# Kernel tuning notes

Hardware: AMD Instinct MI355X
Metric: run time of the kernel (lower is better)

Reference implementation:

```python
import jax, jax.numpy as jnp
import numpy as np


def setup_inputs() -> dict:
    key = jax.random.key(0)
    k1, k2, k3 = jax.random.split(key, 3)
    B, S_enc, S_dec, D = 8, 4096, 4096, 128
    b = jax.random.normal(k1, (B, S_enc, D), dtype=jnp.float32)
    h = jax.random.normal(k2, (B, S_dec, D), dtype=jnp.float32)
    W_b = jax.random.normal(k3, (D, D), dtype=jnp.float32) * (1.0 / np.sqrt(D))
    return {"b": b, "h": h, "W_b": W_b}


def reference(b, h, W_b):
    # tmp1 = h @ W_b : [B, S_dec, D]
    tmp1 = jnp.einsum('btd,de->bte', h, W_b)
    # scores = tmp1 @ b^T : [B, S_dec, S_enc]
    scores = jnp.einsum('bte,bse->bts', tmp1, b)
    attn = jax.nn.softmax(scores, axis=-1)
    # weighted sum over encoder positions (the original does this via a huge
    # tile/broadcast/multiply/reduce_sum; math is a batched matmul)
    cxt = jnp.einsum('bts,bsd->btd', attn, b)
    return cxt
```

## Files before the change

### kernel.cpp

```cpp
#include <hip/hip_runtime.h>

typedef _Float16 half2v __attribute__((ext_vector_type(2)));
typedef _Float16 half4 __attribute__((ext_vector_type(4)));
typedef _Float16 half8 __attribute__((ext_vector_type(8)));
typedef float floatx4 __attribute__((ext_vector_type(4)));

#define B_   8
#define SE   4096
#define SD   4096
#define D_   128
#define NT   64
#define LDB  136
#define LOG2E 1.44269504f

__device__ __forceinline__ void cp16_async(const _Float16* g, _Float16* l) {
    __builtin_amdgcn_global_load_lds((const __attribute__((address_space(1))) unsigned int*)g,
                                     (__attribute__((address_space(3))) unsigned int*)l, 16, 0, 0);
}

__global__ __launch_bounds__(256) void wprep(const float* __restrict__ W,
                                             _Float16* __restrict__ W16,
                                             _Float16* __restrict__ Wlo) {
    int i = blockIdx.x * 256 + threadIdx.x;
    float w = W[i];
    _Float16 hi = (_Float16)w;
    W16[i] = hi;
    Wlo[i] = (_Float16)(w - (float)hi);
}

__global__ __launch_bounds__(256) void kvprep(const float* __restrict__ b,
                                              const _Float16* __restrict__ W16,
                                              const _Float16* __restrict__ Wlo,
                                              _Float16* __restrict__ kp,
                                              _Float16* __restrict__ vT) {
    __shared__ _Float16 bs[64 * LDB];
    const int bb = blockIdx.y, s0 = blockIdx.x * 64;
    const int tid = threadIdx.x, wave = tid >> 6, lane = tid & 63;
    const int l15 = lane & 15, quad = lane >> 4;

    const float* bg = b + ((size_t)bb * SE + s0) * D_;
    #pragma unroll
    for (int it = 0; it < 4; ++it) {
        int idx = tid + it * 256;
        int row = idx >> 4, seg = idx & 15;
        const float* src = bg + row * D_ + seg * 8;
        float4 a = *(const float4*)src;
        float4 c = *(const float4*)(src + 4);
        half8 hv;
        hv[0] = (_Float16)a.x; hv[1] = (_Float16)a.y; hv[2] = (_Float16)a.z; hv[3] = (_Float16)a.w;
        hv[4] = (_Float16)c.x; hv[5] = (_Float16)c.y; hv[6] = (_Float16)c.z; hv[7] = (_Float16)c.w;
        *(half8*)(bs + row * LDB + seg * 8) = hv;
    }
    __syncthreads();

    half8 af[4];
    #pragma unroll
    for (int ks = 0; ks < 4; ++ks)
        af[ks] = *(const half8*)(bs + (wave * 16 + l15) * LDB + ks * 32 + quad * 8);
    floatx4 acc[8];
    #pragma unroll
    for (int nt = 0; nt < 8; ++nt) acc[nt] = (floatx4){0.f, 0.f, 0.f, 0.f};
    #pragma unroll
    for (int ks = 0; ks < 4; ++ks) {
        #pragma unroll
        for (int nt = 0; nt < 8; ++nt) {
            half8 bh = *(const half8*)(W16 + (size_t)(nt * 16 + l15) * 128 + ks * 32 + quad * 8);
            half8 bl = *(const half8*)(Wlo + (size_t)(nt * 16 + l15) * 128 + ks * 32 + quad * 8);
            acc[nt] = __builtin_amdgcn_mfma_f32_16x16x32_f16(af[ks], bh, acc[nt], 0, 0, 0);
            acc[nt] = __builtin_amdgcn_mfma_f32_16x16x32_f16(af[ks], bl, acc[nt], 0, 0, 0);
        }
    }

    {
        const int sq = tid & 15, dg = tid >> 4;
        half8 rowv[4];
        #pragma unroll
        for (int j = 0; j < 4; ++j)
            rowv[j] = *(const half8*)(bs + (sq * 4 + j) * LDB + dg * 8);
        #pragma unroll
        for (int r = 0; r < 8; ++r) {
            int d = dg * 8 + r;
            half4 o;
            #pragma unroll
            for (int j = 0; j < 4; ++j) o[j] = rowv[j][r];
            *(half4*)(vT + ((size_t)bb * D_ + d) * SE + s0 + sq * 4) = o;
        }
    }
    __syncthreads();

    #pragma unroll
    for (int nt = 0; nt < 8; ++nt)
        #pragma unroll
        for (int r = 0; r < 4; ++r)
            bs[(wave * 16 + quad * 4 + r) * LDB + nt * 16 + l15] = (_Float16)acc[nt][r];
    __syncthreads();
    _Float16* kg = kp + ((size_t)bb * SE + s0) * D_;
    {
        const int row = tid >> 2;
        #pragma unroll
        for (int it = 0; it < 4; ++it) {
            int ch = (tid & 3) + it * 4;
            half8 v = *(const half8*)(bs + row * LDB + ch * 8);
            *(half8*)(kg + row * D_ + ch * 8) = v;
        }
    }
}

__global__ __launch_bounds__(256, 2) void flash(const float* __restrict__ h,
                                                const _Float16* __restrict__ k,
                                                const _Float16* __restrict__ vT,
                                                float* __restrict__ out) {
    __shared__ _Float16 KV[2][16384];

    const int bb   = blockIdx.y;
    const int q0   = blockIdx.x * 64;
    const int tid  = threadIdx.x;
    const int wave = tid >> 6;
    const int wq   = wave >> 1;
    const int ws   = wave & 1;
    const int lane = tid & 63;
    const int l15  = lane & 15;
    const int quad = lane >> 4;

    const _Float16* kbase = k + (size_t)bb * SE * D_;
    const _Float16* vbase = vT + (size_t)bb * D_ * SE;

    int koff[4], voff[4];
    #pragma unroll
    for (int j = 0; j < 4; ++j) {
        int i = (wave * 4 + j) * 64 + lane;
        int kr = i >> 4, kpp = i & 15;
        koff[j] = kr * D_ + (kpp ^ (kr & 15)) * 8;
        int vr = i >> 3, vpp = i & 7;
        voff[j] = vr * SE + (vpp ^ (vr & 7)) * 8;
    }

    const _Float16* kA0[4]; const _Float16* kA1[4];
    const _Float16* vB0[2]; const _Float16* vB1[2];
    #pragma unroll
    for (int ks = 0; ks < 4; ++ks) {
        int o = l15 * 128 + (((ks * 4 + quad) ^ l15) * 8) + ws * 4096;
        kA0[ks] = &KV[0][o]; kA1[ks] = &KV[1][o];
    }
    #pragma unroll
    for (int stl = 0; stl < 2; ++stl) {
        int o = 8192 + l15 * 64 + (((ws * 4 + stl * 2 + (quad >> 1)) ^ (l15 & 7)) * 8) + (quad & 1) * 4;
        vB0[stl] = &KV[0][o]; vB1[stl] = &KV[1][o];
    }

    {
        _Float16* buf0 = &KV[0][0];
        #pragma unroll
        for (int j = 0; j < 4; ++j) {
            cp16_async(kbase + koff[j], buf0 + (wave * 4 + j) * 512);
            cp16_async(vbase + voff[j], buf0 + 8192 + (wave * 4 + j) * 512);
        }
    }

    half8 qf[2][4];
    #pragma unroll
    for (int qt = 0; qt < 2; ++qt) {
        const float* hrow = h + ((size_t)bb * SD + q0 + wq * 32 + qt * 16 + l15) * D_;
        #pragma unroll
        for (int ks = 0; ks < 4; ++ks) {
            float4 a = *(const float4*)(hrow + ks * 32 + quad * 8);
            float4 c = *(const float4*)(hrow + ks * 32 + quad * 8 + 4);
            half8 f;
            f[0] = (_Float16)(a.x * LOG2E); f[1] = (_Float16)(a.y * LOG2E);
            f[2] = (_Float16)(a.z * LOG2E); f[3] = (_Float16)(a.w * LOG2E);
            f[4] = (_Float16)(c.x * LOG2E); f[5] = (_Float16)(c.y * LOG2E);
            f[6] = (_Float16)(c.z * LOG2E); f[7] = (_Float16)(c.w * LOG2E);
            qf[qt][ks] = f;
        }
    }

    floatx4 acc_o[2][8];
    #pragma unroll
    for (int qt = 0; qt < 2; ++qt)
        #pragma unroll
        for (int dt = 0; dt < 8; ++dt) acc_o[qt][dt] = (floatx4){0.f, 0.f, 0.f, 0.f};
    float m_q[2] = {-1e30f, -1e30f};
    float l_part[2] = {0.f, 0.f};
    const half2v one2 = { (_Float16)1.f, (_Float16)1.f };

    for (int t = 0; t < SE / NT; ++t) {
        __syncthreads();
        if (t + 1 < SE / NT) {
            const _Float16* kt = kbase + (size_t)(t + 1) * (NT * D_);
            const _Float16* vt = vbase + (size_t)(t + 1) * NT;
            _Float16* bufn = &KV[(t + 1) & 1][0];
            #pragma unroll
            for (int j = 0; j < 4; ++j) {
                cp16_async(kt + koff[j], bufn + (wave * 4 + j) * 512);
                cp16_async(vt + voff[j], bufn + 8192 + (wave * 4 + j) * 512);
            }
        }
        const bool odd = (t & 1) != 0;
        const _Float16* kA[4]; const _Float16* vB[2];
        #pragma unroll
        for (int i = 0; i < 4; ++i) kA[i] = odd ? kA1[i] : kA0[i];
        #pragma unroll
        for (int i = 0; i < 2; ++i) vB[i] = odd ? vB1[i] : vB0[i];

        floatx4 accs[2][2];
        #pragma unroll
        for (int stl = 0; stl < 2; ++stl)
            #pragma unroll
            for (int qt = 0; qt < 2; ++qt) accs[stl][qt] = (floatx4){0.f, 0.f, 0.f, 0.f};
        #pragma unroll
        for (int ks = 0; ks < 4; ++ks) {
            half8 af0 = *(const half8*)(kA[ks]);
            half8 af1 = *(const half8*)(kA[ks] + 2048);
            accs[0][0] = __builtin_amdgcn_mfma_f32_16x16x32_f16(af0, qf[0][ks], accs[0][0], 0, 0, 0);
            accs[0][1] = __builtin_amdgcn_mfma_f32_16x16x32_f16(af0, qf[1][ks], accs[0][1], 0, 0, 0);
            accs[1][0] = __builtin_amdgcn_mfma_f32_16x16x32_f16(af1, qf[0][ks], accs[1][0], 0, 0, 0);
            accs[1][1] = __builtin_amdgcn_mfma_f32_16x16x32_f16(af1, qf[1][ks], accs[1][1], 0, 0, 0);
        }

        float mv[2];
        #pragma unroll
        for (int qt = 0; qt < 2; ++qt) {
            float a = fmaxf(fmaxf(accs[0][qt][0], accs[0][qt][1]), fmaxf(accs[0][qt][2], accs[0][qt][3]));
            float b2 = fmaxf(fmaxf(accs[1][qt][0], accs[1][qt][1]), fmaxf(accs[1][qt][2], accs[1][qt][3]));
            mv[qt] = fmaxf(a, b2);
        }
        bool cond = (mv[0] > m_q[0] + 11.5f) || (mv[1] > m_q[1] + 11.5f);
        if (__ballot(cond) != 0ull) {
            #pragma unroll
            for (int qt = 0; qt < 2; ++qt) {
                float m = mv[qt];
                m = fmaxf(m, __shfl_xor(m, 16, 64));
                m = fmaxf(m, __shfl_xor(m, 32, 64));
                float mnew = fmaxf(m_q[qt], m);
                float alpha = exp2f(m_q[qt] - mnew);
                l_part[qt] *= alpha;
                float ab[4];
                #pragma unroll
                for (int r = 0; r < 4; ++r) ab[r] = __shfl(alpha, quad * 4 + r, 64);
                #pragma unroll
                for (int dt = 0; dt < 8; ++dt)
                    #pragma unroll
                    for (int r = 0; r < 4; ++r) acc_o[qt][dt][r] *= ab[r];
                m_q[qt] = mnew;
            }
        }

        half4 pf[2][2];
        #pragma unroll
        for (int qt = 0; qt < 2; ++qt)
            #pragma unroll
            for (int stl = 0; stl < 2; ++stl) {
                float p0 = exp2f(accs[stl][qt][0] - m_q[qt]);
                float p1 = exp2f(accs[stl][qt][1] - m_q[qt]);
                float p2 = exp2f(accs[stl][qt][2] - m_q[qt]);
                float p3 = exp2f(accs[stl][qt][3] - m_q[qt]);
                half2v lo = __builtin_bit_cast(half2v, __builtin_amdgcn_cvt_pkrtz(p0, p1));
                half2v hi = __builtin_bit_cast(half2v, __builtin_amdgcn_cvt_pkrtz(p2, p3));
#if __has_builtin(__builtin_amdgcn_fdot2)
                l_part[qt] = __builtin_amdgcn_fdot2(lo, one2, l_part[qt], false);
                l_part[qt] = __builtin_amdgcn_fdot2(hi, one2, l_part[qt], false);
#else
                l_part[qt] += p0 + p1 + p2 + p3;
#endif
                half4 pv; pv[0] = lo[0]; pv[1] = lo[1]; pv[2] = hi[0]; pv[3] = hi[1];
                pf[qt][stl] = pv;
            }

        #pragma unroll
        for (int stl = 0; stl < 2; ++stl) {
            #pragma unroll
            for (int dt = 0; dt < 8; ++dt) {
                half4 vf = *(const half4*)(vB[stl] + dt * 1024);
                acc_o[0][dt] = __builtin_amdgcn_mfma_f32_16x16x16f16(pf[0][stl], vf, acc_o[0][dt], 0, 0, 0);
                acc_o[1][dt] = __builtin_amdgcn_mfma_f32_16x16x16f16(pf[1][stl], vf, acc_o[1][dt], 0, 0, 0);
            }
        }
    }

    float l_own[2];
    #pragma unroll
    for (int qt = 0; qt < 2; ++qt) {
        float l = l_part[qt];
        l += __shfl_xor(l, 16, 64);
        l += __shfl_xor(l, 32, 64);
        l_own[qt] = l;
    }

    __syncthreads();
    float* Ob = (float*)&KV[0][0];
    float* ml = (float*)&KV[0][0] + 8192;

    if (ws == 1) {
        #pragma unroll
        for (int qt = 0; qt < 2; ++qt) {
            #pragma unroll
            for (int dt = 0; dt < 8; ++dt)
                *(floatx4*)(Ob + (((wq * 2 + qt) * 8 + dt) * 64 + lane) * 4) = acc_o[qt][dt];
            if (quad == 0)
                *(float2*)(ml + (wq * 32 + qt * 16 + l15) * 2) = make_float2(m_q[qt], l_own[qt]);
        }
    }
    __syncthreads();
    if (ws == 0) {
        #pragma unroll
        for (int qt = 0; qt < 2; ++qt) {
            float m0r[4], l0r[4], m1r[4], l1r[4];
            #pragma unroll
            for (int r = 0; r < 4; ++r) {
                m0r[r] = __shfl(m_q[qt], quad * 4 + r, 64);
                l0r[r] = __shfl(l_own[qt], quad * 4 + r, 64);
                float2 p = *(float2*)(ml + (wq * 32 + qt * 16 + quad * 4 + r) * 2);
                m1r[r] = p.x; l1r[r] = p.y;
            }
            float a0[4], a1[4], inv[4];
            #pragma unroll
            for (int r = 0; r < 4; ++r) {
                float mm = fmaxf(m0r[r], m1r[r]);
                a0[r] = exp2f(m0r[r] - mm);
                a1[r] = exp2f(m1r[r] - mm);
                inv[r] = 1.f / (l0r[r] * a0[r] + l1r[r] * a1[r]);
            }
            float* orow = out + ((size_t)bb * SD + q0 + wq * 32 + qt * 16 + quad * 4) * D_;
            #pragma unroll
            for (int dt = 0; dt < 8; ++dt) {
                floatx4 o1 = *(floatx4*)(Ob + (((wq * 2 + qt) * 8 + dt) * 64 + lane) * 4);
                #pragma unroll
                for (int r = 0; r < 4; ++r)
                    orow[(size_t)r * D_ + dt * 16 + l15] =
                        (acc_o[qt][dt][r] * a0[r] + o1[r] * a1[r]) * inv[r];
            }
        }
    }
}

extern "C" void kernel_launch(void* const* d_in, const int* in_sizes, int n_in,
                              void* d_out, int out_size, void* d_ws, size_t ws_size,
                              hipStream_t stream) {
    const float* b = (const float*)d_in[0];
    const float* h = (const float*)d_in[1];
    const float* W = (const float*)d_in[2];
    float* out = (float*)d_out;

    _Float16* W16 = (_Float16*)d_ws;
    _Float16* Wlo = W16 + 128 * 128;
    _Float16* kp  = Wlo + 128 * 128;
    _Float16* vT  = kp + (size_t)B_ * SE * D_;

    wprep<<<64, 256, 0, stream>>>(W, W16, Wlo);
    kvprep<<<dim3(SE / 64, B_), 256, 0, stream>>>(b, W16, Wlo, kp, vT);
    flash<<<dim3(SD / 64, B_), 256, 0, stream>>>(h, kp, vT, out);
}
```

Measured before the change: 215.9 us.

## Use 512-thread flash blocks with one 16-row query tile per wave

Restructures the flash kernel so each block runs 8 waves, with each wave owning a single 16-row query tile instead of two. Register state per wave drops (acc_o, qf, m/l), so more waves can be resident, and the K/V tile loads are split across twice as many threads. The cost is that each K/V fragment read from LDS now feeds only one query tile instead of two, doubling LDS read traffic per MFMA. The block barrier also has to synchronize 8 waves.

```diff
diff --git a/kernel.cpp b/kernel.cpp
--- a/kernel.cpp
+++ b/kernel.cpp
@@ -106,7 +106,7 @@
     }
 }
 
-__global__ __launch_bounds__(256, 2) void flash(const float* __restrict__ h,
+__global__ __launch_bounds__(512, 4) void flash(const float* __restrict__ h,
                                                 const _Float16* __restrict__ k,
                                                 const _Float16* __restrict__ vT,
                                                 float* __restrict__ out) {
@@ -125,14 +125,14 @@
     const _Float16* kbase = k + (size_t)bb * SE * D_;
     const _Float16* vbase = vT + (size_t)bb * D_ * SE;
 
-    int koff[4], voff[4];
-    #pragma unroll
-    for (int j = 0; j < 4; ++j) {
-        int i = (wave * 4 + j) * 64 + lane;
+    int koff[2], voff[2];
+    #pragma unroll
+    for (int it = 0; it < 2; ++it) {
+        int i = it * 512 + wave * 64 + lane;
         int kr = i >> 4, kpp = i & 15;
-        koff[j] = kr * D_ + (kpp ^ (kr & 15)) * 8;
+        koff[it] = kr * D_ + (kpp ^ (kr & 15)) * 8;
         int vr = i >> 3, vpp = i & 7;
-        voff[j] = vr * SE + (vpp ^ (vr & 7)) * 8;
+        voff[it] = vr * SE + (vpp ^ (vr & 7)) * 8;
     }
 
     const _Float16* kA0[4]; const _Float16* kA1[4];
@@ -151,16 +151,15 @@
     {
         _Float16* buf0 = &KV[0][0];
         #pragma unroll
-        for (int j = 0; j < 4; ++j) {
-            cp16_async(kbase + koff[j], buf0 + (wave * 4 + j) * 512);
-            cp16_async(vbase + voff[j], buf0 + 8192 + (wave * 4 + j) * 512);
-        }
-    }
-
-    half8 qf[2][4];
-    #pragma unroll
-    for (int qt = 0; qt < 2; ++qt) {
-        const float* hrow = h + ((size_t)bb * SD + q0 + wq * 32 + qt * 16 + l15) * D_;
+        for (int it = 0; it < 2; ++it) {
+            cp16_async(kbase + koff[it], buf0 + (it * 512 + wave * 64) * 8);
+            cp16_async(vbase + voff[it], buf0 + 8192 + (it * 512 + wave * 64) * 8);
+        }
+    }
+
+    half8 qf[4];
+    {
+        const float* hrow = h + ((size_t)bb * SD + q0 + wq * 16 + l15) * D_;
         #pragma unroll
         for (int ks = 0; ks < 4; ++ks) {
             float4 a = *(const float4*)(hrow + ks * 32 + quad * 8);
@@ -170,17 +169,15 @@
             f[2] = (_Float16)(a.z * LOG2E); f[3] = (_Float16)(a.w * LOG2E);
             f[4] = (_Float16)(c.x * LOG2E); f[5] = (_Float16)(c.y * LOG2E);
             f[6] = (_Float16)(c.z * LOG2E); f[7] = (_Float16)(c.w * LOG2E);
-            qf[qt][ks] = f;
-        }
-    }
-
-    floatx4 acc_o[2][8];
-    #pragma unroll
-    for (int qt = 0; qt < 2; ++qt)
-        #pragma unroll
-        for (int dt = 0; dt < 8; ++dt) acc_o[qt][dt] = (floatx4){0.f, 0.f, 0.f, 0.f};
-    float m_q[2] = {-1e30f, -1e30f};
-    float l_part[2] = {0.f, 0.f};
+            qf[ks] = f;
+        }
+    }
+
+    floatx4 acc_o[8];
+    #pragma unroll
+    for (int dt = 0; dt < 8; ++dt) acc_o[dt] = (floatx4){0.f, 0.f, 0.f, 0.f};
+    float m_q = -1e30f;
+    float l_part = 0.f;
     const half2v one2 = { (_Float16)1.f, (_Float16)1.f };
 
     for (int t = 0; t < SE / NT; ++t) {
@@ -190,145 +187,121 @@
             const _Float16* vt = vbase + (size_t)(t + 1) * NT;
             _Float16* bufn = &KV[(t + 1) & 1][0];
             #pragma unroll
-            for (int j = 0; j < 4; ++j) {
-                cp16_async(kt + koff[j], bufn + (wave * 4 + j) * 512);
-                cp16_async(vt + voff[j], bufn + 8192 + (wave * 4 + j) * 512);
+            for (int it = 0; it < 2; ++it) {
+                cp16_async(kt + koff[it], bufn + (it * 512 + wave * 64) * 8);
+                cp16_async(vt + voff[it], bufn + 8192 + (it * 512 + wave * 64) * 8);
             }
         }
         const bool odd = (t & 1) != 0;
-        const _Float16* kA[4]; const _Float16* vB[2];
-        #pragma unroll
-        for (int i = 0; i < 4; ++i) kA[i] = odd ? kA1[i] : kA0[i];
-        #pragma unroll
-        for (int i = 0; i < 2; ++i) vB[i] = odd ? vB1[i] : vB0[i];
-
-        floatx4 accs[2][2];
-        #pragma unroll
-        for (int stl = 0; stl < 2; ++stl)
-            #pragma unroll
-            for (int qt = 0; qt < 2; ++qt) accs[stl][qt] = (floatx4){0.f, 0.f, 0.f, 0.f};
+        const _Float16* vB[2];
+        vB[0] = odd ? vB1[0] : vB0[0];
+        vB[1] = odd ? vB1[1] : vB0[1];
+
+        floatx4 accs[2];
+        accs[0] = (floatx4){0.f, 0.f, 0.f, 0.f};
+        accs[1] = (floatx4){0.f, 0.f, 0.f, 0.f};
         #pragma unroll
         for (int ks = 0; ks < 4; ++ks) {
-            half8 af0 = *(const half8*)(kA[ks]);
-            half8 af1 = *(const half8*)(kA[ks] + 2048);
-            accs[0][0] = __builtin_amdgcn_mfma_f32_16x16x32_f16(af0, qf[0][ks], accs[0][0], 0, 0, 0);
-            accs[0][1] = __builtin_amdgcn_mfma_f32_16x16x32_f16(af0, qf[1][ks], accs[0][1], 0, 0, 0);
-            accs[1][0] = __builtin_amdgcn_mfma_f32_16x16x32_f16(af1, qf[0][ks], accs[1][0], 0, 0, 0);
-            accs[1][1] = __builtin_amdgcn_mfma_f32_16x16x32_f16(af1, qf[1][ks], accs[1][1], 0, 0, 0);
-        }
-
-        float mv[2];
-        #pragma unroll
-        for (int qt = 0; qt < 2; ++qt) {
-            float a = fmaxf(fmaxf(accs[0][qt][0], accs[0][qt][1]), fmaxf(accs[0][qt][2], accs[0][qt][3]));
-            float b2 = fmaxf(fmaxf(accs[1][qt][0], accs[1][qt][1]), fmaxf(accs[1][qt][2], accs[1][qt][3]));
-            mv[qt] = fmaxf(a, b2);
-        }
-        bool cond = (mv[0] > m_q[0] + 11.5f) || (mv[1] > m_q[1] + 11.5f);
-        if (__ballot(cond) != 0ull) {
-            #pragma unroll
-            for (int qt = 0; qt < 2; ++qt) {
-                float m = mv[qt];
-                m = fmaxf(m, __shfl_xor(m, 16, 64));
-                m = fmaxf(m, __shfl_xor(m, 32, 64));
-                float mnew = fmaxf(m_q[qt], m);
-                float alpha = exp2f(m_q[qt] - mnew);
-                l_part[qt] *= alpha;
-                float ab[4];
+            const _Float16* ka = odd ? kA1[ks] : kA0[ks];
+            half8 af0 = *(const half8*)(ka);
+            half8 af1 = *(const half8*)(ka + 2048);
+            accs[0] = __builtin_amdgcn_mfma_f32_16x16x32_f16(af0, qf[ks], accs[0], 0, 0, 0);
+            accs[1] = __builtin_amdgcn_mfma_f32_16x16x32_f16(af1, qf[ks], accs[1], 0, 0, 0);
+        }
+
+        float mv = fmaxf(fmaxf(fmaxf(accs[0][0], accs[0][1]), fmaxf(accs[0][2], accs[0][3])),
+                         fmaxf(fmaxf(accs[1][0], accs[1][1]), fmaxf(accs[1][2], accs[1][3])));
+        if (__ballot(mv > m_q + 11.5f) != 0ull) {
+            float m = mv;
+            m = fmaxf(m, __shfl_xor(m, 16, 64));
+            m = fmaxf(m, __shfl_xor(m, 32, 64));
+            float mnew = fmaxf(m_q, m);
+            float alpha = exp2f(m_q - mnew);
+            l_part *= alpha;
+            float ab[4];
+            #pragma unroll
+            for (int r = 0; r < 4; ++r) ab[r] = __shfl(alpha, quad * 4 + r, 64);
+            #pragma unroll
+            for (int dt = 0; dt < 8; ++dt)
                 #pragma unroll
-                for (int r = 0; r < 4; ++r) ab[r] = __shfl(alpha, quad * 4 + r, 64);
-                #pragma unroll
-                for (int dt = 0; dt < 8; ++dt)
-                    #pragma unroll
-                    for (int r = 0; r < 4; ++r) acc_o[qt][dt][r] *= ab[r];
-                m_q[qt] = mnew;
-            }
-        }
-
-        half4 pf[2][2];
-        #pragma unroll
-        for (int qt = 0; qt < 2; ++qt)
-            #pragma unroll
-            for (int stl = 0; stl < 2; ++stl) {
-                float p0 = exp2f(accs[stl][qt][0] - m_q[qt]);
-                float p1 = exp2f(accs[stl][qt][1] - m_q[qt]);
-                float p2 = exp2f(accs[stl][qt][2] - m_q[qt]);
-                float p3 = exp2f(accs[stl][qt][3] - m_q[qt]);
-                half2v lo = __builtin_bit_cast(half2v, __builtin_amdgcn_cvt_pkrtz(p0, p1));
-                half2v hi = __builtin_bit_cast(half2v, __builtin_amdgcn_cvt_pkrtz(p2, p3));
+                for (int r = 0; r < 4; ++r) acc_o[dt][r] *= ab[r];
+            m_q = mnew;
+        }
+
+        half4 pf[2];
+        #pragma unroll
+        for (int stl = 0; stl < 2; ++stl) {
+            float p0 = exp2f(accs[stl][0] - m_q);
+            float p1 = exp2f(accs[stl][1] - m_q);
+            float p2 = exp2f(accs[stl][2] - m_q);
+            float p3 = exp2f(accs[stl][3] - m_q);
+            half2v lo = __builtin_bit_cast(half2v, __builtin_amdgcn_cvt_pkrtz(p0, p1));
+            half2v hi = __builtin_bit_cast(half2v, __builtin_amdgcn_cvt_pkrtz(p2, p3));
 #if __has_builtin(__builtin_amdgcn_fdot2)
-                l_part[qt] = __builtin_amdgcn_fdot2(lo, one2, l_part[qt], false);
-                l_part[qt] = __builtin_amdgcn_fdot2(hi, one2, l_part[qt], false);
+            l_part = __builtin_amdgcn_fdot2(lo, one2, l_part, false);
+            l_part = __builtin_amdgcn_fdot2(hi, one2, l_part, false);
 #else
-                l_part[qt] += p0 + p1 + p2 + p3;
+            l_part += p0 + p1 + p2 + p3;
 #endif
-                half4 pv; pv[0] = lo[0]; pv[1] = lo[1]; pv[2] = hi[0]; pv[3] = hi[1];
-                pf[qt][stl] = pv;
-            }
+            half4 pv; pv[0] = lo[0]; pv[1] = lo[1]; pv[2] = hi[0]; pv[3] = hi[1];
+            pf[stl] = pv;
+        }
 
         #pragma unroll
         for (int stl = 0; stl < 2; ++stl) {
             #pragma unroll
             for (int dt = 0; dt < 8; ++dt) {
                 half4 vf = *(const half4*)(vB[stl] + dt * 1024);
-                acc_o[0][dt] = __builtin_amdgcn_mfma_f32_16x16x16f16(pf[0][stl], vf, acc_o[0][dt], 0, 0, 0);
-                acc_o[1][dt] = __builtin_amdgcn_mfma_f32_16x16x16f16(pf[1][stl], vf, acc_o[1][dt], 0, 0, 0);
+                acc_o[dt] = __builtin_amdgcn_mfma_f32_16x16x16f16(pf[stl], vf, acc_o[dt], 0, 0, 0);
             }
         }
     }
 
-    float l_own[2];
-    #pragma unroll
-    for (int qt = 0; qt < 2; ++qt) {
-        float l = l_part[qt];
+    float l_own;
+    {
+        float l = l_part;
         l += __shfl_xor(l, 16, 64);
         l += __shfl_xor(l, 32, 64);
-        l_own[qt] = l;
+        l_own = l;
     }
 
     __syncthreads();
     float* Ob = (float*)&KV[0][0];
-    float* ml = (float*)&KV[0][0] + 8192;
+    float* ml = (float*)&KV[1][0];
 
     if (ws == 1) {
         #pragma unroll
-        for (int qt = 0; qt < 2; ++qt) {
-            #pragma unroll
-            for (int dt = 0; dt < 8; ++dt)
-                *(floatx4*)(Ob + (((wq * 2 + qt) * 8 + dt) * 64 + lane) * 4) = acc_o[qt][dt];
-            if (quad == 0)
-                *(float2*)(ml + (wq * 32 + qt * 16 + l15) * 2) = make_float2(m_q[qt], l_own[qt]);
-        }
+        for (int dt = 0; dt < 8; ++dt)
+            *(floatx4*)(Ob + ((wq * 8 + dt) * 64 + lane) * 4) = acc_o[dt];
+        if (quad == 0)
+            *(float2*)(ml + (wq * 16 + l15) * 2) = make_float2(m_q, l_own);
     }
     __syncthreads();
     if (ws == 0) {
-        #pragma unroll
-        for (int qt = 0; qt < 2; ++qt) {
-            float m0r[4], l0r[4], m1r[4], l1r[4];
-            #pragma unroll
-            for (int r = 0; r < 4; ++r) {
-                m0r[r] = __shfl(m_q[qt], quad * 4 + r, 64);
-                l0r[r] = __shfl(l_own[qt], quad * 4 + r, 64);
-                float2 p = *(float2*)(ml + (wq * 32 + qt * 16 + quad * 4 + r) * 2);
-                m1r[r] = p.x; l1r[r] = p.y;
-            }
-            float a0[4], a1[4], inv[4];
-            #pragma unroll
-            for (int r = 0; r < 4; ++r) {
-                float mm = fmaxf(m0r[r], m1r[r]);
-                a0[r] = exp2f(m0r[r] - mm);
-                a1[r] = exp2f(m1r[r] - mm);
-                inv[r] = 1.f / (l0r[r] * a0[r] + l1r[r] * a1[r]);
-            }
-            float* orow = out + ((size_t)bb * SD + q0 + wq * 32 + qt * 16 + quad * 4) * D_;
-            #pragma unroll
-            for (int dt = 0; dt < 8; ++dt) {
-                floatx4 o1 = *(floatx4*)(Ob + (((wq * 2 + qt) * 8 + dt) * 64 + lane) * 4);
-                #pragma unroll
-                for (int r = 0; r < 4; ++r)
-                    orow[(size_t)r * D_ + dt * 16 + l15] =
-                        (acc_o[qt][dt][r] * a0[r] + o1[r] * a1[r]) * inv[r];
-            }
+        float m0r[4], l0r[4], m1r[4], l1r[4];
+        #pragma unroll
+        for (int r = 0; r < 4; ++r) {
+            m0r[r] = __shfl(m_q, quad * 4 + r, 64);
+            l0r[r] = __shfl(l_own, quad * 4 + r, 64);
+            float2 p = *(float2*)(ml + (wq * 16 + quad * 4 + r) * 2);
+            m1r[r] = p.x; l1r[r] = p.y;
+        }
+        float a0[4], a1[4], inv[4];
+        #pragma unroll
+        for (int r = 0; r < 4; ++r) {
+            float mm = fmaxf(m0r[r], m1r[r]);
+            a0[r] = exp2f(m0r[r] - mm);
+            a1[r] = exp2f(m1r[r] - mm);
+            inv[r] = 1.f / (l0r[r] * a0[r] + l1r[r] * a1[r]);
+        }
+        float* orow = out + ((size_t)bb * SD + q0 + wq * 16 + quad * 4) * D_;
+        #pragma unroll
+        for (int dt = 0; dt < 8; ++dt) {
+            floatx4 o1 = *(floatx4*)(Ob + ((wq * 8 + dt) * 64 + lane) * 4);
+            #pragma unroll
+            for (int r = 0; r < 4; ++r)
+                orow[(size_t)r * D_ + dt * 16 + l15] =
+                    (acc_o[dt][r] * a0[r] + o1[r] * a1[r]) * inv[r];
         }
     }
 }
@@ -348,5 +321,5 @@
 
     wprep<<<64, 256, 0, stream>>>(W, W16, Wlo);
     kvprep<<<dim3(SE / 64, B_), 256, 0, stream>>>(b, W16, Wlo, kp, vT);
-    flash<<<dim3(SD / 64, B_), 256, 0, stream>>>(h, kp, vT, out);
-}
+    flash<<<dim3(SD / 64, B_), 512, 0, stream>>>(h, kp, vT, out);
+}
```

Measured after the change: 208.5 us. 3.4% less time.

## Split each KV tile across four waves per query group with 512-thread blocks

Applied to the files above, without the earlier changes.

The flash kernel moves from 256 to 512 threads per block, and each query group's 64-key tile is now split across four waves of 16 keys each instead of two waves of 32. Per-wave work per iteration halves, and more waves are available to hide latency and overlap MFMA with the exp/softmax work. The final merge now combines four partial softmax states through shared memory, processed one query subtile at a time, which adds more barriers and a larger reduction. Launch bounds of (512, 4) constrain registers per thread, which the 2x8 output accumulators may strain.

```diff
diff --git a/kernel.cpp b/kernel.cpp
--- a/kernel.cpp
+++ b/kernel.cpp
@@ -106,18 +106,19 @@
     }
 }
 
-__global__ __launch_bounds__(256, 2) void flash(const float* __restrict__ h,
+__global__ __launch_bounds__(512, 4) void flash(const float* __restrict__ h,
                                                 const _Float16* __restrict__ k,
                                                 const _Float16* __restrict__ vT,
                                                 float* __restrict__ out) {
     __shared__ _Float16 KV[2][16384];
+    __shared__ float mlbuf[2][4][16][2];
 
     const int bb   = blockIdx.y;
     const int q0   = blockIdx.x * 64;
     const int tid  = threadIdx.x;
     const int wave = tid >> 6;
-    const int wq   = wave >> 1;
-    const int ws   = wave & 1;
+    const int wq   = wave >> 2;
+    const int ws   = wave & 3;
     const int lane = tid & 63;
     const int l15  = lane & 15;
     const int quad = lane >> 4;
@@ -125,35 +126,34 @@
     const _Float16* kbase = k + (size_t)bb * SE * D_;
     const _Float16* vbase = vT + (size_t)bb * D_ * SE;
 
-    int koff[4], voff[4];
-    #pragma unroll
-    for (int j = 0; j < 4; ++j) {
-        int i = (wave * 4 + j) * 64 + lane;
+    int koff[2], voff[2];
+    #pragma unroll
+    for (int it = 0; it < 2; ++it) {
+        int i = it * 512 + wave * 64 + lane;
         int kr = i >> 4, kpp = i & 15;
-        koff[j] = kr * D_ + (kpp ^ (kr & 15)) * 8;
+        koff[it] = kr * D_ + (kpp ^ (kr & 15)) * 8;
         int vr = i >> 3, vpp = i & 7;
-        voff[j] = vr * SE + (vpp ^ (vr & 7)) * 8;
+        voff[it] = vr * SE + (vpp ^ (vr & 7)) * 8;
     }
 
     const _Float16* kA0[4]; const _Float16* kA1[4];
-    const _Float16* vB0[2]; const _Float16* vB1[2];
+    const _Float16* vB0;    const _Float16* vB1;
     #pragma unroll
     for (int ks = 0; ks < 4; ++ks) {
-        int o = l15 * 128 + (((ks * 4 + quad) ^ l15) * 8) + ws * 4096;
+        int o = (ws * 16 + l15) * 128 + (((ks * 4 + quad) ^ l15) * 8);
         kA0[ks] = &KV[0][o]; kA1[ks] = &KV[1][o];
     }
-    #pragma unroll
-    for (int stl = 0; stl < 2; ++stl) {
-        int o = 8192 + l15 * 64 + (((ws * 4 + stl * 2 + (quad >> 1)) ^ (l15 & 7)) * 8) + (quad & 1) * 4;
-        vB0[stl] = &KV[0][o]; vB1[stl] = &KV[1][o];
+    {
+        int o = 8192 + l15 * 64 + (((2 * ws + (quad >> 1)) ^ (l15 & 7)) * 8) + (quad & 1) * 4;
+        vB0 = &KV[0][o]; vB1 = &KV[1][o];
     }
 
     {
         _Float16* buf0 = &KV[0][0];
         #pragma unroll
-        for (int j = 0; j < 4; ++j) {
-            cp16_async(kbase + koff[j], buf0 + (wave * 4 + j) * 512);
-            cp16_async(vbase + voff[j], buf0 + 8192 + (wave * 4 + j) * 512);
+        for (int it = 0; it < 2; ++it) {
+            cp16_async(kbase + koff[it], buf0 + (it * 512 + wave * 64) * 8);
+            cp16_async(vbase + voff[it], buf0 + 8192 + (it * 512 + wave * 64) * 8);
         }
     }
 
@@ -190,40 +190,28 @@
             const _Float16* vt = vbase + (size_t)(t + 1) * NT;
             _Float16* bufn = &KV[(t + 1) & 1][0];
             #pragma unroll
-            for (int j = 0; j < 4; ++j) {
-                cp16_async(kt + koff[j], bufn + (wave * 4 + j) * 512);
-                cp16_async(vt + voff[j], bufn + 8192 + (wave * 4 + j) * 512);
+            for (int it = 0; it < 2; ++it) {
+                cp16_async(kt + koff[it], bufn + (it * 512 + wave * 64) * 8);
+                cp16_async(vt + voff[it], bufn + 8192 + (it * 512 + wave * 64) * 8);
             }
         }
         const bool odd = (t & 1) != 0;
-        const _Float16* kA[4]; const _Float16* vB[2];
-        #pragma unroll
-        for (int i = 0; i < 4; ++i) kA[i] = odd ? kA1[i] : kA0[i];
-        #pragma unroll
-        for (int i = 0; i < 2; ++i) vB[i] = odd ? vB1[i] : vB0[i];
-
-        floatx4 accs[2][2];
-        #pragma unroll
-        for (int stl = 0; stl < 2; ++stl)
-            #pragma unroll
-            for (int qt = 0; qt < 2; ++qt) accs[stl][qt] = (floatx4){0.f, 0.f, 0.f, 0.f};
+        const _Float16* vB = odd ? vB1 : vB0;
+
+        floatx4 accs[2];
+        accs[0] = (floatx4){0.f, 0.f, 0.f, 0.f};
+        accs[1] = (floatx4){0.f, 0.f, 0.f, 0.f};
         #pragma unroll
         for (int ks = 0; ks < 4; ++ks) {
-            half8 af0 = *(const half8*)(kA[ks]);
-            half8 af1 = *(const half8*)(kA[ks] + 2048);
-            accs[0][0] = __builtin_amdgcn_mfma_f32_16x16x32_f16(af0, qf[0][ks], accs[0][0], 0, 0, 0);
-            accs[0][1] = __builtin_amdgcn_mfma_f32_16x16x32_f16(af0, qf[1][ks], accs[0][1], 0, 0, 0);
-            accs[1][0] = __builtin_amdgcn_mfma_f32_16x16x32_f16(af1, qf[0][ks], accs[1][0], 0, 0, 0);
-            accs[1][1] = __builtin_amdgcn_mfma_f32_16x16x32_f16(af1, qf[1][ks], accs[1][1], 0, 0, 0);
+            half8 af = *(const half8*)(odd ? kA1[ks] : kA0[ks]);
+            accs[0] = __builtin_amdgcn_mfma_f32_16x16x32_f16(af, qf[0][ks], accs[0], 0, 0, 0);
+            accs[1] = __builtin_amdgcn_mfma_f32_16x16x32_f16(af, qf[1][ks], accs[1], 0, 0, 0);
         }
 
         float mv[2];
         #pragma unroll
-        for (int qt = 0; qt < 2; ++qt) {
-            float a = fmaxf(fmaxf(accs[0][qt][0], accs[0][qt][1]), fmaxf(accs[0][qt][2], accs[0][qt][3]));
-            float b2 = fmaxf(fmaxf(accs[1][qt][0], accs[1][qt][1]), fmaxf(accs[1][qt][2], accs[1][qt][3]));
-            mv[qt] = fmaxf(a, b2);
-        }
+        for (int qt = 0; qt < 2; ++qt)
+            mv[qt] = fmaxf(fmaxf(accs[qt][0], accs[qt][1]), fmaxf(accs[qt][2], accs[qt][3]));
         bool cond = (mv[0] > m_q[0] + 11.5f) || (mv[1] > m_q[1] + 11.5f);
         if (__ballot(cond) != 0ull) {
             #pragma unroll
@@ -245,35 +233,30 @@
             }
         }
 
-        half4 pf[2][2];
-        #pragma unroll
-        for (int qt = 0; qt < 2; ++qt)
-            #pragma unroll
-            for (int stl = 0; stl < 2; ++stl) {
-                float p0 = exp2f(accs[stl][qt][0] - m_q[qt]);
-                float p1 = exp2f(accs[stl][qt][1] - m_q[qt]);
-                float p2 = exp2f(accs[stl][qt][2] - m_q[qt]);
-                float p3 = exp2f(accs[stl][qt][3] - m_q[qt]);
-                half2v lo = __builtin_bit_cast(half2v, __builtin_amdgcn_cvt_pkrtz(p0, p1));
-                half2v hi = __builtin_bit_cast(half2v, __builtin_amdgcn_cvt_pkrtz(p2, p3));
+        half4 pf[2];
+        #pragma unroll
+        for (int qt = 0; qt < 2; ++qt) {
+            float p0 = exp2f(accs[qt][0] - m_q[qt]);
+            float p1 = exp2f(accs[qt][1] - m_q[qt]);
+            float p2 = exp2f(accs[qt][2] - m_q[qt]);
+            float p3 = exp2f(accs[qt][3] - m_q[qt]);
+            half2v lo = __builtin_bit_cast(half2v, __builtin_amdgcn_cvt_pkrtz(p0, p1));
+            half2v hi = __builtin_bit_cast(half2v, __builtin_amdgcn_cvt_pkrtz(p2, p3));
 #if __has_builtin(__builtin_amdgcn_fdot2)
-                l_part[qt] = __builtin_amdgcn_fdot2(lo, one2, l_part[qt], false);
-                l_part[qt] = __builtin_amdgcn_fdot2(hi, one2, l_part[qt], false);
+            l_part[qt] = __builtin_amdgcn_fdot2(lo, one2, l_part[qt], false);
+            l_part[qt] = __builtin_amdgcn_fdot2(hi, one2, l_part[qt], false);
 #else
-                l_part[qt] += p0 + p1 + p2 + p3;
+            l_part[qt] += p0 + p1 + p2 + p3;
 #endif
-                half4 pv; pv[0] = lo[0]; pv[1] = lo[1]; pv[2] = hi[0]; pv[3] = hi[1];
-                pf[qt][stl] = pv;
-            }
-
-        #pragma unroll
-        for (int stl = 0; stl < 2; ++stl) {
-            #pragma unroll
-            for (int dt = 0; dt < 8; ++dt) {
-                half4 vf = *(const half4*)(vB[stl] + dt * 1024);
-                acc_o[0][dt] = __builtin_amdgcn_mfma_f32_16x16x16f16(pf[0][stl], vf, acc_o[0][dt], 0, 0, 0);
-                acc_o[1][dt] = __builtin_amdgcn_mfma_f32_16x16x16f16(pf[1][stl], vf, acc_o[1][dt], 0, 0, 0);
-            }
+            half4 pv; pv[0] = lo[0]; pv[1] = lo[1]; pv[2] = hi[0]; pv[3] = hi[1];
+            pf[qt] = pv;
+        }
+
+        #pragma unroll
+        for (int dt = 0; dt < 8; ++dt) {
+            half4 vf = *(const half4*)(vB + dt * 1024);
+            acc_o[0][dt] = __builtin_amdgcn_mfma_f32_16x16x16f16(pf[0], vf, acc_o[0][dt], 0, 0, 0);
+            acc_o[1][dt] = __builtin_amdgcn_mfma_f32_16x16x16f16(pf[1], vf, acc_o[1][dt], 0, 0, 0);
         }
     }
 
@@ -286,48 +269,52 @@
         l_own[qt] = l;
     }
 
-    __syncthreads();
     float* Ob = (float*)&KV[0][0];
-    float* ml = (float*)&KV[0][0] + 8192;
-
-    if (ws == 1) {
-        #pragma unroll
-        for (int qt = 0; qt < 2; ++qt) {
+
+    #pragma unroll
+    for (int qt = 0; qt < 2; ++qt) {
+        __syncthreads();
+        if (ws != 0) {
+            float* reg = Ob + (wq * 3 + (ws - 1)) * 2048;
             #pragma unroll
             for (int dt = 0; dt < 8; ++dt)
-                *(floatx4*)(Ob + (((wq * 2 + qt) * 8 + dt) * 64 + lane) * 4) = acc_o[qt][dt];
-            if (quad == 0)
-                *(float2*)(ml + (wq * 32 + qt * 16 + l15) * 2) = make_float2(m_q[qt], l_own[qt]);
-        }
-    }
-    __syncthreads();
-    if (ws == 0) {
-        #pragma unroll
-        for (int qt = 0; qt < 2; ++qt) {
-            float m0r[4], l0r[4], m1r[4], l1r[4];
+                *(floatx4*)(reg + (dt * 64 + lane) * 4) = acc_o[qt][dt];
+            if (quad == 0) {
+                mlbuf[wq][ws][l15][0] = m_q[qt];
+                mlbuf[wq][ws][l15][1] = l_own[qt];
+            }
+        }
+        __syncthreads();
+        if (ws == 0) {
+            float m0 = m_q[qt],           l0 = l_own[qt];
+            float m1 = mlbuf[wq][1][l15][0], l1 = mlbuf[wq][1][l15][1];
+            float m2 = mlbuf[wq][2][l15][0], l2 = mlbuf[wq][2][l15][1];
+            float m3 = mlbuf[wq][3][l15][0], l3 = mlbuf[wq][3][l15][1];
+            float mm = fmaxf(fmaxf(m0, m1), fmaxf(m2, m3));
+            float a0 = exp2f(m0 - mm), a1 = exp2f(m1 - mm);
+            float a2 = exp2f(m2 - mm), a3 = exp2f(m3 - mm);
+            float linv = 1.f / (l0 * a0 + l1 * a1 + l2 * a2 + l3 * a3);
+            float a0b[4], a1b[4], a2b[4], a3b[4], lb[4];
             #pragma unroll
             for (int r = 0; r < 4; ++r) {
-                m0r[r] = __shfl(m_q[qt], quad * 4 + r, 64);
-                l0r[r] = __shfl(l_own[qt], quad * 4 + r, 64);
-                float2 p = *(float2*)(ml + (wq * 32 + qt * 16 + quad * 4 + r) * 2);
-                m1r[r] = p.x; l1r[r] = p.y;
-            }
-            float a0[4], a1[4], inv[4];
-            #pragma unroll
-            for (int r = 0; r < 4; ++r) {
-                float mm = fmaxf(m0r[r], m1r[r]);
-                a0[r] = exp2f(m0r[r] - mm);
-                a1[r] = exp2f(m1r[r] - mm);
-                inv[r] = 1.f / (l0r[r] * a0[r] + l1r[r] * a1[r]);
+                int src = quad * 4 + r;
+                a0b[r] = __shfl(a0, src, 64);
+                a1b[r] = __shfl(a1, src, 64);
+                a2b[r] = __shfl(a2, src, 64);
+                a3b[r] = __shfl(a3, src, 64);
+                lb[r]  = __shfl(linv, src, 64);
             }
             float* orow = out + ((size_t)bb * SD + q0 + wq * 32 + qt * 16 + quad * 4) * D_;
             #pragma unroll
             for (int dt = 0; dt < 8; ++dt) {
-                floatx4 o1 = *(floatx4*)(Ob + (((wq * 2 + qt) * 8 + dt) * 64 + lane) * 4);
+                floatx4 o1 = *(floatx4*)(Ob + (wq * 3 + 0) * 2048 + (dt * 64 + lane) * 4);
+                floatx4 o2 = *(floatx4*)(Ob + (wq * 3 + 1) * 2048 + (dt * 64 + lane) * 4);
+                floatx4 o3 = *(floatx4*)(Ob + (wq * 3 + 2) * 2048 + (dt * 64 + lane) * 4);
                 #pragma unroll
                 for (int r = 0; r < 4; ++r)
                     orow[(size_t)r * D_ + dt * 16 + l15] =
-                        (acc_o[qt][dt][r] * a0[r] + o1[r] * a1[r]) * inv[r];
+                        (acc_o[qt][dt][r] * a0b[r] + o1[r] * a1b[r]
+                         + o2[r] * a2b[r] + o3[r] * a3b[r]) * lb[r];
             }
         }
     }
@@ -348,5 +335,5 @@
 
     wprep<<<64, 256, 0, stream>>>(W, W16, Wlo);
     kvprep<<<dim3(SE / 64, B_), 256, 0, stream>>>(b, W16, Wlo, kp, vT);
-    flash<<<dim3(SD / 64, B_), 256, 0, stream>>>(h, kp, vT, out);
-}
+    flash<<<dim3(SD / 64, B_), 512, 0, stream>>>(h, kp, vT, out);
+}
```

New measurement: 278.5 us. 29.0% more time.
